# Optimization experiments

Hardware: AMD Instinct MI355X
Metric: run time of the kernel (lower is better)

Reference implementation:

```python
import jax, jax.numpy as jnp
import numpy as np

N_HEAD = 16
N_EMBD = 2048


def _rope(x):
    # x: (B, H, L, D). FAITHFUL to source: _apply_rope unpacks (B, L, H, D) on a
    # (B, H, L, D) tensor, so rotation angle = head_index * inv_freq, broadcast over
    # all sequence positions (a latent bug in the original, reproduced exactly).
    B, H, L, D = x.shape
    inv_freq = 1.0 / (10000.0 ** (jnp.arange(0, D, 2, dtype=jnp.float32) / D))  # (D/2,)
    theta = jnp.arange(H, dtype=jnp.float32)[:, None] * inv_freq[None, :]       # (H, D/2)
    cos = jnp.cos(theta)[None, :, None, :]  # (1, H, 1, D/2)
    sin = jnp.sin(theta)[None, :, None, :]
    xp = x.astype(jnp.float32).reshape(B, H, L, D // 2, 2)
    x0, x1 = xp[..., 0], xp[..., 1]
    r0 = x0 * cos - x1 * sin
    r1 = x0 * sin + x1 * cos
    return jnp.stack([r0, r1], axis=-1).reshape(B, H, L, D).astype(x.dtype)


def setup_inputs() -> dict:
    key = jax.random.key(0)
    k1, k2, k3 = jax.random.split(key, 3)
    B, L, C = 2, 2048, N_EMBD
    s = 1.0 / np.sqrt(C).astype(np.float32)
    x = jax.random.normal(k1, (B, L, C), dtype=jnp.float32)
    w_attn = jax.random.normal(k2, (3 * C, C), dtype=jnp.float32) * s
    w_proj = jax.random.normal(k3, (C, C), dtype=jnp.float32) * s
    return {"x": x, "w_attn": w_attn, "w_proj": w_proj}


def reference(x, w_attn, w_proj):
    B, L, C = x.shape
    H = N_HEAD
    D = C // H
    qkv = x @ w_attn.T                       # (B, L, 3C)
    q, k, v = jnp.split(qkv, 3, axis=2)
    q = q.reshape(B, L, H, D).transpose(0, 2, 1, 3)  # (B, H, L, D)
    k = k.reshape(B, L, H, D).transpose(0, 2, 1, 3)
    v = v.reshape(B, L, H, D).transpose(0, 2, 1, 3)
    q = _rope(q)
    k = _rope(k)
    attn = jnp.einsum('bhqd,bhkd->bhqk', q, k) * (1.0 / np.sqrt(D).astype(np.float32))
    causal = jnp.tril(jnp.ones((L, L), dtype=bool))
    attn = jnp.where(causal[None, None], attn, -jnp.inf)
    attn = jax.nn.softmax(attn, axis=-1)
    y = jnp.einsum('bhqk,bhkd->bhqd', attn, v)
    y = y.transpose(0, 2, 1, 3).reshape(B, L, C)
    return y @ w_proj.T
```

## Files before the change

kernel.cpp:

```cpp
#include <hip/hip_runtime.h>

typedef __attribute__((ext_vector_type(8))) short bf16x8;
typedef __attribute__((ext_vector_type(4))) float f32x4;

__device__ __forceinline__ unsigned short f2bf(float f) {
  unsigned int u = __float_as_uint(f);
  u += 0x7FFF + ((u >> 16) & 1);
  return (unsigned short)(u >> 16);
}

__device__ __forceinline__ void gload_lds16(const void* g, void* l) {
  __builtin_amdgcn_global_load_lds(
      (const __attribute__((address_space(1))) unsigned int*)g,
      (__attribute__((address_space(3))) unsigned int*)l,
      16, 0, 0);
}

#define MF(a, b, c) __builtin_amdgcn_mfma_f32_16x16x32_bf16((a), (b), (c), 0, 0, 0)
#define FENCE asm volatile("" ::: "memory")

__global__ void cast_all(const float* __restrict__ x,
                         const float* __restrict__ wa,
                         const float* __restrict__ wp,
                         unsigned short* __restrict__ xb,
                         unsigned short* __restrict__ wab,
                         unsigned short* __restrict__ wpb,
                         int n1, int n2, int n4) {
  int stride = gridDim.x * blockDim.x;
  for (int i = blockIdx.x * blockDim.x + threadIdx.x; i < n4; i += stride) {
    const float4* src;
    ushort4* dst;
    int j;
    if (i < n1)      { src = (const float4*)x,  dst = (ushort4*)xb,  j = i; }
    else if (i < n2) { src = (const float4*)wa, dst = (ushort4*)wab, j = i - n1; }
    else             { src = (const float4*)wp, dst = (ushort4*)wpb, j = i - n2; }
    float4 v = src[j];
    ushort4 o;
    o.x = f2bf(v.x); o.y = f2bf(v.y); o.z = f2bf(v.z); o.w = f2bf(v.w);
    dst[j] = o;
  }
}

template<int EPI>
__global__ __launch_bounds__(512, 2)
void gemm8p(const unsigned short* __restrict__ A,
            const unsigned short* __restrict__ Bw,
            float* __restrict__ Cf,
            unsigned short* __restrict__ Qo,
            unsigned short* __restrict__ Ko,
            unsigned short* __restrict__ Vo,
            int M, int N, int K, int Lseq) {
  __shared__ unsigned short Al[2][128 * 64];
  __shared__ unsigned short Bl[2][256 * 64];
  const int tid = threadIdx.x;
  const int lane = tid & 63, w = tid >> 6;
  const int wm = w >> 2, wn = w & 3;
  const int g4 = lane >> 4, r16 = lane & 15;
  const long arow0 = (long)blockIdx.y * 128;
  const long brow0 = (long)blockIdx.x * 256;

#define LDA(db, mf, ks)                                                       \
  (*(const bf16x8*)((const char*)&Al[db][0] +                                 \
                    ((wm * 64 + (mf)*16 + r16) << 7) +                        \
                    ((((ks)*4 + g4) ^ (r16 & 7)) << 4)))
#define LDB(db, nf, ks)                                                       \
  (*(const bf16x8*)((const char*)&Bl[db][0] +                                 \
                    ((wn * 64 + (nf)*16 + r16) << 7) +                        \
                    ((((ks)*4 + g4) ^ (r16 & 7)) << 4)))

#define STGA(db, kt)                                                          \
  do {                                                                        \
    _Pragma("unroll")                                                         \
    for (int c_ = 0; c_ < 2; ++c_) {                                          \
      int off_ = (c_ << 13) + (tid << 4);                                     \
      int row_ = off_ >> 7;                                                   \
      int cbs_ = ((off_ >> 4) & 7) ^ (row_ & 7);                              \
      gload_lds16(A + (arow0 + row_) * (long)K + ((kt) << 6) + cbs_ * 8,      \
                  (char*)&Al[db][0] + off_);                                  \
    }                                                                         \
  } while (0)
#define STGB(db, kt)                                                          \
  do {                                                                        \
    _Pragma("unroll")                                                         \
    for (int c_ = 0; c_ < 4; ++c_) {                                          \
      int off_ = (c_ << 13) + (tid << 4);                                     \
      int row_ = off_ >> 7;                                                   \
      int cbs_ = ((off_ >> 4) & 7) ^ (row_ & 7);                              \
      gload_lds16(Bw + (brow0 + row_) * (long)K + ((kt) << 6) + cbs_ * 8,     \
                  (char*)&Bl[db][0] + off_);                                  \
    }                                                                         \
  } while (0)

  f32x4 acc[4][4];
#pragma unroll
  for (int i = 0; i < 4; ++i)
#pragma unroll
    for (int j = 0; j < 4; ++j) acc[i][j] = (f32x4){0.f, 0.f, 0.f, 0.f};

  bf16x8 b00, b01, b10, b11, b20, b21, b30, b31;

#define LOADB(db)                                                             \
  do {                                                                        \
    b00 = LDB(db, 0, 0); b01 = LDB(db, 0, 1);                                 \
    b10 = LDB(db, 1, 0); b11 = LDB(db, 1, 1);                                 \
    b20 = LDB(db, 2, 0); b21 = LDB(db, 2, 1);                                 \
    b30 = LDB(db, 3, 0); b31 = LDB(db, 3, 1);                                 \
  } while (0)

#define PH(db, q, STAGE_STMT, VMSTMT)                                         \
  do {                                                                        \
    bf16x8 a00 = LDA(db, 2*(q), 0), a01 = LDA(db, 2*(q), 1);                  \
    bf16x8 a10 = LDA(db, 2*(q)+1, 0), a11 = LDA(db, 2*(q)+1, 1);              \
    STAGE_STMT;                                                               \
    VMSTMT;                                                                   \
    FENCE; __builtin_amdgcn_s_barrier(); FENCE;                               \
    __builtin_amdgcn_s_setprio(1);                                            \
    acc[2*(q)][0] = MF(a00, b00, acc[2*(q)][0]);                              \
    acc[2*(q)][0] = MF(a01, b01, acc[2*(q)][0]);                              \
    acc[2*(q)][1] = MF(a00, b10, acc[2*(q)][1]);                              \
    acc[2*(q)][1] = MF(a01, b11, acc[2*(q)][1]);                              \
    acc[2*(q)][2] = MF(a00, b20, acc[2*(q)][2]);                              \
    acc[2*(q)][2] = MF(a01, b21, acc[2*(q)][2]);                              \
    acc[2*(q)][3] = MF(a00, b30, acc[2*(q)][3]);                              \
    acc[2*(q)][3] = MF(a01, b31, acc[2*(q)][3]);                              \
    acc[2*(q)+1][0] = MF(a10, b00, acc[2*(q)+1][0]);                          \
    acc[2*(q)+1][0] = MF(a11, b01, acc[2*(q)+1][0]);                          \
    acc[2*(q)+1][1] = MF(a10, b10, acc[2*(q)+1][1]);                          \
    acc[2*(q)+1][1] = MF(a11, b11, acc[2*(q)+1][1]);                          \
    acc[2*(q)+1][2] = MF(a10, b20, acc[2*(q)+1][2]);                          \
    acc[2*(q)+1][2] = MF(a11, b21, acc[2*(q)+1][2]);                          \
    acc[2*(q)+1][3] = MF(a10, b30, acc[2*(q)+1][3]);                          \
    acc[2*(q)+1][3] = MF(a11, b31, acc[2*(q)+1][3]);                          \
    __builtin_amdgcn_s_setprio(0);                                            \
    FENCE; __builtin_amdgcn_s_barrier(); FENCE;                               \
  } while (0)

#define VM4 asm volatile("s_waitcnt vmcnt(4)" ::: "memory")

  const int NT = K >> 6;
  STGB(0, 0); STGA(0, 0); STGB(1, 1);
  VM4;
  FENCE; __builtin_amdgcn_s_barrier(); FENCE;

  for (int i = 0; i < (NT >> 1); ++i) {
    const int t1 = 2 * i + 1;
    int t2 = 2 * i + 2; if (t2 > NT - 1) t2 = NT - 1;
    int t3 = 2 * i + 3; if (t3 > NT - 1) t3 = NT - 1;
    LOADB(0);
    PH(0, 0, STGA(1, t1), );
    PH(0, 1, STGB(0, t2), VM4);
    LOADB(1);
    PH(1, 0, STGA(0, t2), );
    PH(1, 1, STGB(1, t3), VM4);
  }
  asm volatile("s_waitcnt vmcnt(0)" ::: "memory");

  const float qscale = 0.08838834764831845f;
#pragma unroll
  for (int mf = 0; mf < 4; ++mf) {
#pragma unroll
    for (int nf = 0; nf < 4; ++nf) {
#pragma unroll
      for (int i = 0; i < 4; ++i) {
        long row = arow0 + wm * 64 + mf * 16 + 4 * g4 + i;
        long col = brow0 + wn * 64 + nf * 16 + r16;
        float v = acc[mf][nf][i];
        if (EPI == 0) {
          Cf[row * N + col] = v;
        } else {
          int which = (int)(col >> 11);
          int h = ((int)col >> 7) & 15;
          int d = (int)col & 127;
          int b = (int)(row >> 11);
          int l = (int)row & 2047;
          long bhead = (long)(b * 16 + h);
          if (which == 0)
            Qo[(bhead * Lseq + l) * 128 + d] = f2bf(v * qscale);
          else if (which == 1)
            Ko[(bhead * Lseq + l) * 128 + d] = f2bf(v);
          else
            Vo[(bhead * 128 + d) * Lseq + l] = f2bf(v);
        }
      }
    }
  }
#undef LDA
#undef LDB
#undef STGA
#undef STGB
#undef PH
#undef LOADB
#undef VM4
}

template<int EPI>
__global__ __launch_bounds__(256, 4)
void gemm_bt(const unsigned short* __restrict__ A,
             const unsigned short* __restrict__ Bw,
             float* __restrict__ Cf,
             unsigned short* __restrict__ Qo,
             unsigned short* __restrict__ Ko,
             unsigned short* __restrict__ Vo,
             int M, int N, int K, int Lseq, int nbx) {
  __shared__ unsigned short As[2][128 * 32];
  __shared__ unsigned short Bs[2][128 * 32];
  const int tid = threadIdx.x;
  const int lane = tid & 63, w = tid >> 6;
  const int wm = w >> 1, wn = w & 1;
  const int g4 = lane >> 4, r16 = lane & 15;

  const int nwg = gridDim.x;
  const int cpx = nwg >> 3;
  const int bid = (blockIdx.x & 7) * cpx + (blockIdx.x >> 3);
  const long arow0 = (long)(bid / nbx) * 128;
  const long brow0 = (long)(bid % nbx) * 128;

#define STAGE_G(k0_, buf_)                                                    \
  do {                                                                        \
    _Pragma("unroll")                                                         \
    for (int c_ = 0; c_ < 2; ++c_) {                                          \
      int off_ = (w << 11) + (c_ << 10) + (lane << 4);                        \
      int row_ = off_ >> 6;                                                   \
      int cbs_ = ((off_ >> 4) & 3) ^ ((row_ >> 1) & 3);                       \
      gload_lds16(A + (arow0 + row_) * (long)K + (k0_) + cbs_ * 8,            \
                  (char*)As[buf_] + off_);                                    \
      gload_lds16(Bw + (brow0 + row_) * (long)K + (k0_) + cbs_ * 8,           \
                  (char*)Bs[buf_] + off_);                                    \
    }                                                                         \
  } while (0)

  f32x4 acc[4][4];
#pragma unroll
  for (int i = 0; i < 4; ++i)
#pragma unroll
    for (int j = 0; j < 4; ++j) acc[i][j] = (f32x4){0.f, 0.f, 0.f, 0.f};

  const int T = K >> 5;
  int cur = 0;
  STAGE_G(0, 0);

  for (int t = 0; t < T; ++t) {
    if (t < T - 1) {
      STAGE_G((t + 1) << 5, cur ^ 1);
      asm volatile("s_waitcnt vmcnt(4)" ::: "memory");
    } else {
      asm volatile("s_waitcnt vmcnt(0)" ::: "memory");
    }
    __builtin_amdgcn_s_barrier();

    const int rb = g4 ^ ((r16 >> 1) & 3);
    bf16x8 af[4], bf[4];
#pragma unroll
    for (int mf = 0; mf < 4; ++mf)
      af[mf] = *(const bf16x8*)((const char*)As[cur] +
                                ((64 * wm + 16 * mf + r16) << 6) + (rb << 4));
#pragma unroll
    for (int nf = 0; nf < 4; ++nf)
      bf[nf] = *(const bf16x8*)((const char*)Bs[cur] +
                                ((64 * wn + 16 * nf + r16) << 6) + (rb << 4));
#pragma unroll
    for (int mf = 0; mf < 4; ++mf)
#pragma unroll
      for (int nf = 0; nf < 4; ++nf)
        acc[mf][nf] = MF(af[mf], bf[nf], acc[mf][nf]);
    asm volatile("" ::: "memory");
    __builtin_amdgcn_s_barrier();
    cur ^= 1;
  }
#undef STAGE_G

  const float qscale = 0.08838834764831845f;
#pragma unroll
  for (int mf = 0; mf < 4; ++mf) {
#pragma unroll
    for (int nf = 0; nf < 4; ++nf) {
#pragma unroll
      for (int i = 0; i < 4; ++i) {
        long row = arow0 + 64 * wm + 16 * mf + 4 * g4 + i;
        long col = brow0 + 64 * wn + 16 * nf + r16;
        float v = acc[mf][nf][i];
        if (EPI == 0) {
          Cf[row * N + col] = v;
        } else {
          int which = (int)(col >> 11);
          int h = ((int)col >> 7) & 15;
          int d = (int)col & 127;
          int b = (int)(row >> 11);
          int l = (int)row & 2047;
          long bhead = (long)(b * 16 + h);
          if (which == 0)
            Qo[(bhead * Lseq + l) * 128 + d] = f2bf(v * qscale);
          else if (which == 1)
            Ko[(bhead * Lseq + l) * 128 + d] = f2bf(v);
          else
            Vo[(bhead * 128 + d) * Lseq + l] = f2bf(v);
        }
      }
    }
  }
}

__global__ __launch_bounds__(256, 2)
void attn_fwd(const unsigned short* __restrict__ Q,
              const unsigned short* __restrict__ K,
              const unsigned short* __restrict__ Vt,
              unsigned short* __restrict__ Y, int L) {
  const int D = 128;
  const int id = blockIdx.x;
  const int g = id & 7, kk = id >> 3;
  const int bh = (g << 2) + (kk >> 5);
  const int qt = 31 - (kk & 31);
  const int tid = threadIdx.x, lane = tid & 63, w = tid >> 6;
  const int g4 = lane >> 4, r16 = lane & 15;
  const int q0 = qt * 64;

  __shared__ unsigned short Klds[2 * 64 * 128];
  __shared__ unsigned short Vlds[2 * 128 * 64];
  __shared__ unsigned short P[4][16][64];
  __shared__ float corrS[4][16];
  __shared__ float lrunS[4][16];

  const unsigned short* Qh = Q + (long)bh * L * D;
  const unsigned short* Kh = K + (long)bh * L * D;
  const unsigned short* Vh = Vt + (long)bh * D * L;

#define STAGE_TILE(kt_, buf_)                                                 \
  do {                                                                        \
    const int kbase_ = (kt_) * 64;                                            \
    _Pragma("unroll")                                                         \
    for (int r_ = 0; r_ < 4; ++r_) {                                          \
      int off_ = (tid << 4) + (r_ << 12);                                     \
      int krow_ = off_ >> 8, kcb_ = (off_ >> 4) & 15;                         \
      int kcbs_ = kcb_ ^ (krow_ & 7);                                         \
      gload_lds16(Kh + (long)(kbase_ + krow_) * 128 + kcbs_ * 8,              \
                  (char*)Klds + (buf_)*16384 + (w << 10) + (r_ << 12));       \
      int vrow_ = off_ >> 7, vcb_ = (off_ >> 4) & 7;                          \
      int vcbs_ = vcb_ ^ (vrow_ & 7);                                         \
      gload_lds16(Vh + (long)vrow_ * L + kbase_ + vcbs_ * 8,                  \
                  (char*)Vlds + (buf_)*16384 + (w << 10) + (r_ << 12));       \
    }                                                                         \
  } while (0)

  bf16x8 qf[4];
  {
    long qrow = q0 + 16 * w + r16;
#pragma unroll
    for (int ks = 0; ks < 4; ++ks)
      qf[ks] = *(const bf16x8*)(Qh + qrow * D + ks * 32 + g4 * 8);
  }
  f32x4 o[8];
#pragma unroll
  for (int j = 0; j < 8; ++j) o[j] = (f32x4){0.f, 0.f, 0.f, 0.f};
  float mrun = -1e30f, lrun = 0.f;
  const int qg = q0 + 16 * w + r16;
  char* Pl = (char*)&P[w][0][0];

  int cur = 0;
  STAGE_TILE(0, 0);

  for (int kt = 0; kt <= qt; ++kt) {
    if (kt < qt) {
      STAGE_TILE(kt + 1, cur ^ 1);
      asm volatile("s_waitcnt vmcnt(8)" ::: "memory");
    } else {
      asm volatile("s_waitcnt vmcnt(0)" ::: "memory");
    }
    __builtin_amdgcn_s_barrier();

    const char* Kl = (const char*)Klds + cur * 16384;
    const char* Vl = (const char*)Vlds + cur * 16384;

    f32x4 s[4];
#pragma unroll
    for (int nf = 0; nf < 4; ++nf) s[nf] = (f32x4){0.f, 0.f, 0.f, 0.f};
#pragma unroll
    for (int ks = 0; ks < 4; ++ks) {
#pragma unroll
      for (int nf = 0; nf < 4; ++nf) {
        int row = 16 * nf + r16;
        bf16x8 kf = *(const bf16x8*)(Kl + row * 256 +
                                     (((ks * 4 + g4) ^ (row & 7)) << 4));
        s[nf] = MF(kf, qf[ks], s[nf]);
      }
    }

    const bool diag = (kt == qt);
    float rmax = -1e30f;
#pragma unroll
    for (int nf = 0; nf < 4; ++nf)
#pragma unroll
      for (int i = 0; i < 4; ++i) {
        float t = s[nf][i];
        if (diag && (kt * 64 + 16 * nf + 4 * g4 + i) > qg) t = -1e30f;
        s[nf][i] = t;
        rmax = fmaxf(rmax, t);
      }
    rmax = fmaxf(rmax, __shfl_xor(rmax, 16));
    rmax = fmaxf(rmax, __shfl_xor(rmax, 32));

    const bool full = __any(rmax > mrun + 8.0f);
    float corr = 1.f;
    if (full) {
      float mnew = fmaxf(mrun, rmax);
      corr = __expf(mrun - mnew);
      mrun = mnew;
      if (g4 == 0) corrS[w][r16] = corr;
    }

    float rs = 0.f;
#pragma unroll
    for (int nf = 0; nf < 4; ++nf) {
      float p0 = __expf(s[nf][0] - mrun);
      float p1 = __expf(s[nf][1] - mrun);
      float p2 = __expf(s[nf][2] - mrun);
      float p3 = __expf(s[nf][3] - mrun);
      rs += (p0 + p1) + (p2 + p3);
      ushort4 pw;
      pw.x = f2bf(p0); pw.y = f2bf(p1); pw.z = f2bf(p2); pw.w = f2bf(p3);
      *(ushort4*)(Pl + r16 * 128 + (((2 * nf + (g4 >> 1)) ^ (r16 & 7)) << 4) +
                  ((g4 & 1) << 3)) = pw;
    }
    rs += __shfl_xor(rs, 16);
    rs += __shfl_xor(rs, 32);
    lrun = lrun * corr + rs;

    if (full) {
#pragma unroll
      for (int i = 0; i < 4; ++i) {
        float cb = corrS[w][4 * g4 + i];
#pragma unroll
        for (int nf2 = 0; nf2 < 8; ++nf2) o[nf2][i] *= cb;
      }
    }

#pragma unroll
    for (int ks2 = 0; ks2 < 2; ++ks2) {
      bf16x8 pf = *(const bf16x8*)(Pl + r16 * 128 +
                                   (((ks2 * 4 + g4) ^ (r16 & 7)) << 4));
#pragma unroll
      for (int nf2 = 0; nf2 < 8; ++nf2) {
        int row = 16 * nf2 + r16;
        bf16x8 vf = *(const bf16x8*)(Vl + row * 128 +
                                     (((ks2 * 4 + g4) ^ (row & 7)) << 4));
        o[nf2] = MF(pf, vf, o[nf2]);
      }
    }
    FENCE;
    __builtin_amdgcn_s_barrier();
    cur ^= 1;
  }
#undef STAGE_TILE

  if (g4 == 0) lrunS[w][r16] = lrun;
  const int b = bh >> 4, h = bh & 15;
#pragma unroll
  for (int i = 0; i < 4; ++i) {
    float linv = 1.f / lrunS[w][4 * g4 + i];
#pragma unroll
    for (int nf2 = 0; nf2 < 8; ++nf2) {
      long row = (long)b * L + q0 + 16 * w + 4 * g4 + i;
      Y[row * 2048 + h * 128 + 16 * nf2 + r16] = f2bf(o[nf2][i] * linv);
    }
  }
}

extern "C" void kernel_launch(void* const* d_in, const int* in_sizes, int n_in,
                              void* d_out, int out_size, void* d_ws,
                              size_t ws_size, hipStream_t stream) {
  const float* x = (const float*)d_in[0];
  const float* wa = (const float*)d_in[1];
  const float* wp = (const float*)d_in[2];
  float* out = (float*)d_out;
  const int B = 2, L = 2048, C = 2048;
  const int M = B * L;

  unsigned short* xb = (unsigned short*)d_ws;
  unsigned short* wab = xb + (size_t)M * C;
  unsigned short* wpb = wab + (size_t)3 * C * C;
  unsigned short* Qb = wpb + (size_t)C * C;
  unsigned short* Kb = Qb + (size_t)M * C;
  unsigned short* Vb = Kb + (size_t)M * C;
  unsigned short* Yb = Vb + (size_t)M * C;

  const int n1 = M * C / 4;
  const int n2 = n1 + 3 * C * C / 4;
  const int n4 = n2 + C * C / 4;
  cast_all<<<2048, 256, 0, stream>>>(x, wa, wp, xb, wab, wpb, n1, n2, n4);

  gemm8p<1><<<dim3(3 * C / 256, M / 128), 512, 0, stream>>>(
      xb, wab, nullptr, Qb, Kb, Vb, M, 3 * C, C, L);

  attn_fwd<<<1024, 256, 0, stream>>>(Qb, Kb, Vb, Yb, L);

  gemm_bt<0><<<(M / 128) * (C / 128), 256, 0, stream>>>(
      Yb, wpb, out, nullptr, nullptr, nullptr, M, C, C, L, C / 128);
}
```

Before: 293.2 us.

## Switch gemm8p to 32x32x16 MFMA with a triple-buffered LDS pipeline

Rewrites the gemm8p main loop to use 32x32x16 bf16 MFMA tiles (2x2 per wave) in place of 16x16x32 tiles, which reduces LDS fragment reads per flop. The double-buffered two-phase schedule becomes a three-stage ring buffer that prefetches two k-tiles ahead, with one barrier pair per k-tile. LDS use grows to three buffers (144KB per block at 512 threads), which may limit occupancy to one block per CU despite the launch_bounds of 2. The epilogue index mapping is updated for the 32x32 accumulator layout.

```diff
diff --git a/kernel.cpp b/kernel.cpp
--- a/kernel.cpp
+++ b/kernel.cpp
@@ -2,6 +2,7 @@
 
 typedef __attribute__((ext_vector_type(8))) short bf16x8;
 typedef __attribute__((ext_vector_type(4))) float f32x4;
+typedef __attribute__((ext_vector_type(16))) float f32x16;
 
 __device__ __forceinline__ unsigned short f2bf(float f) {
   unsigned int u = __float_as_uint(f);
@@ -17,6 +18,7 @@
 }
 
 #define MF(a, b, c) __builtin_amdgcn_mfma_f32_16x16x32_bf16((a), (b), (c), 0, 0, 0)
+#define MF32(a, b, c) __builtin_amdgcn_mfma_f32_32x32x16_bf16((a), (b), (c), 0, 0, 0)
 #define FENCE asm volatile("" ::: "memory")
 
 __global__ void cast_all(const float* __restrict__ x,
@@ -50,25 +52,26 @@
             unsigned short* __restrict__ Ko,
             unsigned short* __restrict__ Vo,
             int M, int N, int K, int Lseq) {
-  __shared__ unsigned short Al[2][128 * 64];
-  __shared__ unsigned short Bl[2][256 * 64];
+  __shared__ unsigned short Al[3][128 * 64];
+  __shared__ unsigned short Bl[3][256 * 64];
   const int tid = threadIdx.x;
   const int lane = tid & 63, w = tid >> 6;
   const int wm = w >> 2, wn = w & 3;
-  const int g4 = lane >> 4, r16 = lane & 15;
+  const int l31 = lane & 31, l5 = lane >> 5;
+  const int sa = l31 & 7;
   const long arow0 = (long)blockIdx.y * 128;
   const long brow0 = (long)blockIdx.x * 256;
 
-#define LDA(db, mf, ks)                                                       \
-  (*(const bf16x8*)((const char*)&Al[db][0] +                                 \
-                    ((wm * 64 + (mf)*16 + r16) << 7) +                        \
-                    ((((ks)*4 + g4) ^ (r16 & 7)) << 4)))
-#define LDB(db, nf, ks)                                                       \
-  (*(const bf16x8*)((const char*)&Bl[db][0] +                                 \
-                    ((wn * 64 + (nf)*16 + r16) << 7) +                        \
-                    ((((ks)*4 + g4) ^ (r16 & 7)) << 4)))
-
-#define STGA(db, kt)                                                          \
+#define LDA32(p, mi, ks)                                                      \
+  (*(const bf16x8*)((const char*)Al + (p)*16384 +                             \
+                    ((wm * 64 + (mi)*32 + l31) << 7) +                        \
+                    ((((ks)*2 + l5) ^ sa) << 4)))
+#define LDB32(p, ni, ks)                                                      \
+  (*(const bf16x8*)((const char*)Bl + (p)*32768 +                             \
+                    ((wn * 64 + (ni)*32 + l31) << 7) +                        \
+                    ((((ks)*2 + l5) ^ sa) << 4)))
+
+#define STGA(pbuf, kt)                                                        \
   do {                                                                        \
     _Pragma("unroll")                                                         \
     for (int c_ = 0; c_ < 2; ++c_) {                                          \
@@ -76,10 +79,10 @@
       int row_ = off_ >> 7;                                                   \
       int cbs_ = ((off_ >> 4) & 7) ^ (row_ & 7);                              \
       gload_lds16(A + (arow0 + row_) * (long)K + ((kt) << 6) + cbs_ * 8,      \
-                  (char*)&Al[db][0] + off_);                                  \
+                  (char*)Al + (pbuf)*16384 + off_);                           \
     }                                                                         \
   } while (0)
-#define STGB(db, kt)                                                          \
+#define STGB(pbuf, kt)                                                        \
   do {                                                                        \
     _Pragma("unroll")                                                         \
     for (int c_ = 0; c_ < 4; ++c_) {                                          \
@@ -87,93 +90,76 @@
       int row_ = off_ >> 7;                                                   \
       int cbs_ = ((off_ >> 4) & 7) ^ (row_ & 7);                              \
       gload_lds16(Bw + (brow0 + row_) * (long)K + ((kt) << 6) + cbs_ * 8,     \
-                  (char*)&Bl[db][0] + off_);                                  \
+                  (char*)Bl + (pbuf)*32768 + off_);                           \
     }                                                                         \
   } while (0)
 
-  f32x4 acc[4][4];
-#pragma unroll
-  for (int i = 0; i < 4; ++i)
-#pragma unroll
-    for (int j = 0; j < 4; ++j) acc[i][j] = (f32x4){0.f, 0.f, 0.f, 0.f};
-
-  bf16x8 b00, b01, b10, b11, b20, b21, b30, b31;
-
-#define LOADB(db)                                                             \
-  do {                                                                        \
-    b00 = LDB(db, 0, 0); b01 = LDB(db, 0, 1);                                 \
-    b10 = LDB(db, 1, 0); b11 = LDB(db, 1, 1);                                 \
-    b20 = LDB(db, 2, 0); b21 = LDB(db, 2, 1);                                 \
-    b30 = LDB(db, 3, 0); b31 = LDB(db, 3, 1);                                 \
-  } while (0)
-
-#define PH(db, q, STAGE_STMT, VMSTMT)                                         \
-  do {                                                                        \
-    bf16x8 a00 = LDA(db, 2*(q), 0), a01 = LDA(db, 2*(q), 1);                  \
-    bf16x8 a10 = LDA(db, 2*(q)+1, 0), a11 = LDA(db, 2*(q)+1, 1);              \
-    STAGE_STMT;                                                               \
-    VMSTMT;                                                                   \
-    FENCE; __builtin_amdgcn_s_barrier(); FENCE;                               \
-    __builtin_amdgcn_s_setprio(1);                                            \
-    acc[2*(q)][0] = MF(a00, b00, acc[2*(q)][0]);                              \
-    acc[2*(q)][0] = MF(a01, b01, acc[2*(q)][0]);                              \
-    acc[2*(q)][1] = MF(a00, b10, acc[2*(q)][1]);                              \
-    acc[2*(q)][1] = MF(a01, b11, acc[2*(q)][1]);                              \
-    acc[2*(q)][2] = MF(a00, b20, acc[2*(q)][2]);                              \
-    acc[2*(q)][2] = MF(a01, b21, acc[2*(q)][2]);                              \
-    acc[2*(q)][3] = MF(a00, b30, acc[2*(q)][3]);                              \
-    acc[2*(q)][3] = MF(a01, b31, acc[2*(q)][3]);                              \
-    acc[2*(q)+1][0] = MF(a10, b00, acc[2*(q)+1][0]);                          \
-    acc[2*(q)+1][0] = MF(a11, b01, acc[2*(q)+1][0]);                          \
-    acc[2*(q)+1][1] = MF(a10, b10, acc[2*(q)+1][1]);                          \
-    acc[2*(q)+1][1] = MF(a11, b11, acc[2*(q)+1][1]);                          \
-    acc[2*(q)+1][2] = MF(a10, b20, acc[2*(q)+1][2]);                          \
-    acc[2*(q)+1][2] = MF(a11, b21, acc[2*(q)+1][2]);                          \
-    acc[2*(q)+1][3] = MF(a10, b30, acc[2*(q)+1][3]);                          \
-    acc[2*(q)+1][3] = MF(a11, b31, acc[2*(q)+1][3]);                          \
-    __builtin_amdgcn_s_setprio(0);                                            \
-    FENCE; __builtin_amdgcn_s_barrier(); FENCE;                               \
-  } while (0)
-
-#define VM4 asm volatile("s_waitcnt vmcnt(4)" ::: "memory")
+#define VM6 asm volatile("s_waitcnt vmcnt(6)" ::: "memory")
+
+  f32x16 acc[2][2];
+#pragma unroll
+  for (int i = 0; i < 2; ++i)
+#pragma unroll
+    for (int j = 0; j < 2; ++j)
+#pragma unroll
+      for (int e = 0; e < 16; ++e) acc[i][j][e] = 0.f;
 
   const int NT = K >> 6;
-  STGB(0, 0); STGA(0, 0); STGB(1, 1);
-  VM4;
+  STGA(0, 0); STGB(0, 0);
+  STGA(1, 1); STGB(1, 1);
+  VM6;
   FENCE; __builtin_amdgcn_s_barrier(); FENCE;
 
-  for (int i = 0; i < (NT >> 1); ++i) {
-    const int t1 = 2 * i + 1;
-    int t2 = 2 * i + 2; if (t2 > NT - 1) t2 = NT - 1;
-    int t3 = 2 * i + 3; if (t3 > NT - 1) t3 = NT - 1;
-    LOADB(0);
-    PH(0, 0, STGA(1, t1), );
-    PH(0, 1, STGB(0, t2), VM4);
-    LOADB(1);
-    PH(1, 0, STGA(0, t2), );
-    PH(1, 1, STGB(1, t3), VM4);
+  int p = 0;
+  for (int t = 0; t < NT; ++t) {
+    int ps = p + 2; if (ps >= 3) ps -= 3;
+    int ts = t + 2; if (ts > NT - 1) ts = NT - 1;
+
+    bf16x8 a[2][4], b[2][4];
+#pragma unroll
+    for (int ks = 0; ks < 4; ++ks) {
+      a[0][ks] = LDA32(p, 0, ks);
+      a[1][ks] = LDA32(p, 1, ks);
+      b[0][ks] = LDB32(p, 0, ks);
+      b[1][ks] = LDB32(p, 1, ks);
+    }
+    STGA(ps, ts); STGB(ps, ts);
+    VM6;
+    FENCE; __builtin_amdgcn_s_barrier(); FENCE;
+    __builtin_amdgcn_s_setprio(1);
+#pragma unroll
+    for (int ks = 0; ks < 4; ++ks) {
+      acc[0][0] = MF32(a[0][ks], b[0][ks], acc[0][0]);
+      acc[0][1] = MF32(a[0][ks], b[1][ks], acc[0][1]);
+      acc[1][0] = MF32(a[1][ks], b[0][ks], acc[1][0]);
+      acc[1][1] = MF32(a[1][ks], b[1][ks], acc[1][1]);
+    }
+    __builtin_amdgcn_s_setprio(0);
+    FENCE; __builtin_amdgcn_s_barrier(); FENCE;
+    ++p; if (p == 3) p = 0;
   }
   asm volatile("s_waitcnt vmcnt(0)" ::: "memory");
 
   const float qscale = 0.08838834764831845f;
 #pragma unroll
-  for (int mf = 0; mf < 4; ++mf) {
-#pragma unroll
-    for (int nf = 0; nf < 4; ++nf) {
-#pragma unroll
-      for (int i = 0; i < 4; ++i) {
-        long row = arow0 + wm * 64 + mf * 16 + 4 * g4 + i;
-        long col = brow0 + wn * 64 + nf * 16 + r16;
-        float v = acc[mf][nf][i];
+  for (int mi = 0; mi < 2; ++mi) {
+#pragma unroll
+    for (int ni = 0; ni < 2; ++ni) {
+#pragma unroll
+      for (int reg = 0; reg < 16; ++reg) {
+        long row = arow0 + wm * 64 + mi * 32 +
+                   (reg & 3) + 8 * (reg >> 2) + 4 * l5;
+        long col = brow0 + wn * 64 + ni * 32 + l31;
+        float v = acc[mi][ni][reg];
         if (EPI == 0) {
           Cf[row * N + col] = v;
         } else {
           int which = (int)(col >> 11);
           int h = ((int)col >> 7) & 15;
           int d = (int)col & 127;
-          int b = (int)(row >> 11);
+          int b_ = (int)(row >> 11);
           int l = (int)row & 2047;
-          long bhead = (long)(b * 16 + h);
+          long bhead = (long)(b_ * 16 + h);
           if (which == 0)
             Qo[(bhead * Lseq + l) * 128 + d] = f2bf(v * qscale);
           else if (which == 1)
@@ -184,13 +170,11 @@
       }
     }
   }
-#undef LDA
-#undef LDB
+#undef LDA32
+#undef LDB32
 #undef STGA
 #undef STGB
-#undef PH
-#undef LOADB
-#undef VM4
+#undef VM6
 }
 
 template<int EPI>
```

Result: slower. 307.8 us (+5.0%).
